# Kernel optimization log

Measured on AMD Instinct MI355X. Metric: run time of the kernel, lower is better.

The kernel has to match this reference:

```python
import jax, jax.numpy as jnp
import numpy as np

VOCAB = 50257
CH = 1024          # c_hidden_size = hidden_size(1020) + class_num(4)
LAT = 128
T = 1024
EOS = 1


def setup_inputs() -> dict:
    key = jax.random.key(0)
    ks = jax.random.split(key, 12)
    s = 0.02
    # tokens in [2, VOCAB) so EOS only appears at the final position
    toks = jax.random.randint(ks[0], (T,), 2, VOCAB, dtype=jnp.int32)
    input_tensor = toks.at[-1].set(EOS)
    inp = {
        "input_tensor": input_tensor,
        "h0": jnp.zeros((1, 1, CH), jnp.float32),
        "c0": jnp.zeros((1, 1, CH), jnp.float32),
        "eps": jax.random.normal(ks[1], (1, 1, LAT), jnp.float32),
        "emb": jax.random.normal(ks[2], (VOCAB, CH), jnp.float32) * s,
        "W_ih": jax.random.normal(ks[3], (4 * CH, CH), jnp.float32) * s,
        "W_hh": jax.random.normal(ks[4], (4 * CH, CH), jnp.float32) * s,
        "b_ih": jax.random.normal(ks[5], (4 * CH,), jnp.float32) * s,
        "b_hh": jax.random.normal(ks[6], (4 * CH,), jnp.float32) * s,
        "W_mean": jax.random.normal(ks[7], (LAT, 2 * CH), jnp.float32) * s,
        "b_mean": jnp.zeros((LAT,), jnp.float32),
        "W_logv": jax.random.normal(ks[8], (LAT, 2 * CH), jnp.float32) * s,
        "b_logv": jnp.zeros((LAT,), jnp.float32),
    }
    return inp


def reference(input_tensor, h0, c0, eps, emb, W_ih, W_hh, b_ih, b_hh,
              W_mean, b_mean, W_logv, b_logv):
    Tlen = input_tensor.shape[0]
    eos_idx = jnp.argmax(input_tensor == EOS)           # first EOS position
    active = jnp.arange(Tlen) < eos_idx                 # steps taken before break
    x_all = emb[input_tensor]                            # [T, CH]

    def step(carry, inp):
        h, c = carry
        x, a = inp
        gates = x @ W_ih.T + b_ih + h @ W_hh.T + b_hh    # [4*CH]
        i, f, g, o = jnp.split(gates, 4)                 # PyTorch LSTM gate order
        c_new = jax.nn.sigmoid(f) * c + jax.nn.sigmoid(i) * jnp.tanh(g)
        h_new = jax.nn.sigmoid(o) * jnp.tanh(c_new)
        h = jnp.where(a, h_new, h)
        c = jnp.where(a, c_new, c)
        return (h, c), None

    (h, c), _ = jax.lax.scan(step, (h0.reshape(-1), c0.reshape(-1)), (x_all, active))
    hc = jnp.concatenate([h, c])                         # cat((h, c), dim=2) flattened
    mean = hc @ W_mean.T + b_mean
    logv = hc @ W_logv.T + b_logv
    z = eps.reshape(-1) * jnp.exp(0.5 * logv) + mean     # reparameterize
    shp = (1, 1, LAT)
    return z.reshape(shp), mean.reshape(shp), logv.reshape(shp)
```

## Files before the change

### kernel.cpp

```cpp
#include <hip/hip_runtime.h>
#include <cstdint>
#include <cstddef>

#define T_LEN 1024
#define CH    1024
#define NGATE 4096
#define LAT   128
#define NBLK  128

#define WS_XG    0
#define WS_HBUF  (16777216)
#define WS_HFIN  (16777216 + 16384)
#define WS_CFIN  (16777216 + 24576)
#define WS_CTRL  (16777216 + 32768)

#define SWZ(i) ((i) ^ ((((i) >> 4) & 7) << 2))

__device__ __forceinline__ float sigmf(float x) { return 1.0f / (1.0f + expf(-x)); }

template <int CTRL, int RM>
__device__ __forceinline__ float dpp_add(float x) {
  int t = __builtin_amdgcn_update_dpp(0, __float_as_int(x), CTRL, RM, 0xf, true);
  return x + __int_as_float(t);
}

__device__ __forceinline__ float wave_sum63(float x) {
  x = dpp_add<0x111, 0xf>(x);
  x = dpp_add<0x112, 0xf>(x);
  x = dpp_add<0x114, 0xf>(x);
  x = dpp_add<0x118, 0xf>(x);
  x = dpp_add<0x142, 0xa>(x);
  x = dpp_add<0x143, 0xc>(x);
  return x;
}

__global__ __launch_bounds__(1024) void setup_k(const int* __restrict__ tok,
                                                int* __restrict__ ctrl) {
  __shared__ int red[1024];
  int tid = threadIdx.x;
  red[tid] = (tok[tid] == 1) ? tid : 0x7fffffff;
  __syncthreads();
  for (int s = 512; s > 0; s >>= 1) {
    if (tid < s) red[tid] = min(red[tid], red[tid + s]);
    __syncthreads();
  }
  if (tid == 0) {
    int e = red[0];
    ctrl[0] = (e == 0x7fffffff) ? 0 : e;
  }
}

__global__ __launch_bounds__(512) void xgemm_k(const int* __restrict__ tok,
                                               const float* __restrict__ emb,
                                               const float* __restrict__ Wih,
                                               const float* __restrict__ bih,
                                               const float* __restrict__ bhh,
                                               float* __restrict__ xg) {
  __shared__ float As[16 * 132];
  __shared__ float Bs[16 * 132];
  const int tid = threadIdx.x;
  const int r0 = blockIdx.x * 128;
  const int t0 = blockIdx.y * 128;
  const int tx = tid & 15, ty = tid >> 4;
  const int m0 = ty * 4, n0 = tx * 8;
  const int lrow = tid >> 2;
  const int kq   = (tid & 3) * 4;

  float acc[4][8];
#pragma unroll
  for (int i = 0; i < 4; i++)
#pragma unroll
    for (int j = 0; j < 8; j++) acc[i][j] = 0.0f;

  const int tokv = tok[t0 + lrow];
  const float* arow = emb + (size_t)tokv * CH;
  const float* brow = Wih + (size_t)(r0 + lrow) * CH;

  for (int k0 = 0; k0 < CH; k0 += 16) {
    float4 a4 = *(const float4*)(arow + k0 + kq);
    float4 b4 = *(const float4*)(brow + k0 + kq);
    __syncthreads();
    As[(kq + 0) * 132 + lrow] = a4.x;
    As[(kq + 1) * 132 + lrow] = a4.y;
    As[(kq + 2) * 132 + lrow] = a4.z;
    As[(kq + 3) * 132 + lrow] = a4.w;
    Bs[(kq + 0) * 132 + lrow] = b4.x;
    Bs[(kq + 1) * 132 + lrow] = b4.y;
    Bs[(kq + 2) * 132 + lrow] = b4.z;
    Bs[(kq + 3) * 132 + lrow] = b4.w;
    __syncthreads();
#pragma unroll
    for (int kk = 0; kk < 16; kk++) {
      float4 av = *(const float4*)&As[kk * 132 + m0];
      float4 b0 = *(const float4*)&Bs[kk * 132 + n0];
      float4 b1 = *(const float4*)&Bs[kk * 132 + n0 + 4];
      float aa[4] = {av.x, av.y, av.z, av.w};
      float bb[8] = {b0.x, b0.y, b0.z, b0.w, b1.x, b1.y, b1.z, b1.w};
#pragma unroll
      for (int i = 0; i < 4; i++)
#pragma unroll
        for (int j = 0; j < 8; j++) acc[i][j] += aa[i] * bb[j];
    }
  }

  float4 bi0 = *(const float4*)(bih + r0 + n0);
  float4 bi1 = *(const float4*)(bih + r0 + n0 + 4);
  float4 bh0 = *(const float4*)(bhh + r0 + n0);
  float4 bh1 = *(const float4*)(bhh + r0 + n0 + 4);
  float badd[8] = {bi0.x + bh0.x, bi0.y + bh0.y, bi0.z + bh0.z, bi0.w + bh0.w,
                   bi1.x + bh1.x, bi1.y + bh1.y, bi1.z + bh1.z, bi1.w + bh1.w};
#pragma unroll
  for (int i = 0; i < 4; i++) {
    float4 o0 = {acc[i][0] + badd[0], acc[i][1] + badd[1],
                 acc[i][2] + badd[2], acc[i][3] + badd[3]};
    float4 o1 = {acc[i][4] + badd[4], acc[i][5] + badd[5],
                 acc[i][6] + badd[6], acc[i][7] + badd[7]};
    float* dst = xg + (size_t)(t0 + m0 + i) * NGATE + r0 + n0;
    *(float4*)(dst) = o0;
    *(float4*)(dst + 4) = o1;
  }
}

__global__ __launch_bounds__(1024) void lstm_k(const float* __restrict__ h0,
                                               const float* __restrict__ c0,
                                               const float* __restrict__ eps,
                                               const float* __restrict__ Whh,
                                               const float* __restrict__ Wm,
                                               const float* __restrict__ bm,
                                               const float* __restrict__ Wl,
                                               const float* __restrict__ bl,
                                               const float* __restrict__ xg,
                                               unsigned long long* __restrict__ hbuf64,
                                               unsigned long long* __restrict__ hfin64,
                                               unsigned long long* __restrict__ cfin64,
                                               const int* __restrict__ ctrl,
                                               float* __restrict__ out) {
  __shared__ float hs[1024];
  __shared__ float hcs[2048];
  __shared__ float4 gpart[16];
  __shared__ float rs[32];

  const int tid = threadIdx.x;
  const int b = blockIdx.x;
  const int wv = tid >> 6;
  const int ln = tid & 63;
  const int dw = wv & 7;
  const int mb = (wv >> 3) * 2;
  const int hsw = SWZ(tid);
  const int swzmask = (ln & 7) << 2;
  const int idx0 = (ln * 16 + 4 * mb) ^ swzmask;
  const int idx1 = (ln * 16 + 4 * mb + 4) ^ swzmask;

  float4 w4[4][2];
#pragma unroll
  for (int q = 0; q < 4; q++) {
    const float* wr = Whh + (size_t)(q * 1024 + b * 8 + dw) * CH + ln * 16 + 4 * mb;
    w4[q][0] = *(const float4*)(wr);
    w4[q][1] = *(const float4*)(wr + 4);
  }

  const int eos = ctrl[0];

  float hreg = 0.0f, creg = 0.0f;
  if (tid < 8) { hreg = h0[b * 8 + tid]; creg = c0[b * 8 + tid]; }

  for (int t = 0; t < eos; t++) {
    float xq0 = 0.0f, xq1 = 0.0f, xq2 = 0.0f, xq3 = 0.0f;
    if (tid < 8) {
      const float* xp = xg + (size_t)t * NGATE + b * 8 + tid;
      xq0 = xp[0]; xq1 = xp[1024]; xq2 = xp[2048]; xq3 = xp[3072];
    }

    if (t == 0) {
      hs[hsw] = h0[tid];
    } else {
      const unsigned want = (unsigned)t;
      const unsigned long long* src = hbuf64 + (size_t)(t & 1) * 1024 + tid;
      unsigned long long v;
      do {
        v = __hip_atomic_load(src, __ATOMIC_RELAXED, __HIP_MEMORY_SCOPE_AGENT);
      } while ((unsigned)(v >> 32) != want);
      hs[hsw] = __uint_as_float((unsigned)(v & 0xffffffffu));
    }
    __syncthreads();

    float a0 = 0.0f, a1 = 0.0f, a2 = 0.0f, a3 = 0.0f;
    {
      const float4 h4a = *(const float4*)&hs[idx0];
      const float4 h4b = *(const float4*)&hs[idx1];
      a0 += w4[0][0].x * h4a.x; a0 += w4[0][0].y * h4a.y;
      a0 += w4[0][0].z * h4a.z; a0 += w4[0][0].w * h4a.w;
      a0 += w4[0][1].x * h4b.x; a0 += w4[0][1].y * h4b.y;
      a0 += w4[0][1].z * h4b.z; a0 += w4[0][1].w * h4b.w;
      a1 += w4[1][0].x * h4a.x; a1 += w4[1][0].y * h4a.y;
      a1 += w4[1][0].z * h4a.z; a1 += w4[1][0].w * h4a.w;
      a1 += w4[1][1].x * h4b.x; a1 += w4[1][1].y * h4b.y;
      a1 += w4[1][1].z * h4b.z; a1 += w4[1][1].w * h4b.w;
      a2 += w4[2][0].x * h4a.x; a2 += w4[2][0].y * h4a.y;
      a2 += w4[2][0].z * h4a.z; a2 += w4[2][0].w * h4a.w;
      a2 += w4[2][1].x * h4b.x; a2 += w4[2][1].y * h4b.y;
      a2 += w4[2][1].z * h4b.z; a2 += w4[2][1].w * h4b.w;
      a3 += w4[3][0].x * h4a.x; a3 += w4[3][0].y * h4a.y;
      a3 += w4[3][0].z * h4a.z; a3 += w4[3][0].w * h4a.w;
      a3 += w4[3][1].x * h4b.x; a3 += w4[3][1].y * h4b.y;
      a3 += w4[3][1].z * h4b.z; a3 += w4[3][1].w * h4b.w;
    }
    a0 = wave_sum63(a0);
    a1 = wave_sum63(a1);
    a2 = wave_sum63(a2);
    a3 = wave_sum63(a3);
    if (ln == 63) gpart[wv] = float4{a0, a1, a2, a3};
    __syncthreads();

    if (tid < 8) {
      const float4 g0 = gpart[tid];
      const float4 g1 = gpart[tid + 8];
      const float iv = g0.x + g1.x + xq0;
      const float fv = g0.y + g1.y + xq1;
      const float gg = g0.z + g1.z + xq2;
      const float ov = g0.w + g1.w + xq3;
      const float cn = sigmf(fv) * creg + sigmf(iv) * tanhf(gg);
      const float hn = sigmf(ov) * tanhf(cn);
      creg = cn; hreg = hn;
      const unsigned long long pv =
          ((unsigned long long)(unsigned)(t + 1) << 32) |
          (unsigned long long)__float_as_uint(hn);
      __hip_atomic_store(&hbuf64[(size_t)((t + 1) & 1) * 1024 + b * 8 + tid], pv,
                         __ATOMIC_RELAXED, __HIP_MEMORY_SCOPE_AGENT);
    }
  }

  if (tid < 8) {
    const unsigned long long ph = (1ull << 32) | (unsigned long long)__float_as_uint(hreg);
    const unsigned long long pc = (1ull << 32) | (unsigned long long)__float_as_uint(creg);
    __hip_atomic_store(&hfin64[b * 8 + tid], ph, __ATOMIC_RELAXED, __HIP_MEMORY_SCOPE_AGENT);
    __hip_atomic_store(&cfin64[b * 8 + tid], pc, __ATOMIC_RELAXED, __HIP_MEMORY_SCOPE_AGENT);
  }

  {
    unsigned long long vh, vc;
    do {
      vh = __hip_atomic_load(&hfin64[tid], __ATOMIC_RELAXED, __HIP_MEMORY_SCOPE_AGENT);
    } while ((unsigned)(vh >> 32) != 1u);
    do {
      vc = __hip_atomic_load(&cfin64[tid], __ATOMIC_RELAXED, __HIP_MEMORY_SCOPE_AGENT);
    } while ((unsigned)(vc >> 32) != 1u);
    hcs[tid] = __uint_as_float((unsigned)(vh & 0xffffffffu));
    hcs[1024 + tid] = __uint_as_float((unsigned)(vc & 0xffffffffu));
  }
  __syncthreads();

  float hc1 = hcs[tid];
  float hc2 = hcs[1024 + tid];
  float pm = Wm[(size_t)b * 2048 + tid] * hc1 + Wm[(size_t)b * 2048 + 1024 + tid] * hc2;
  float pl = Wl[(size_t)b * 2048 + tid] * hc1 + Wl[(size_t)b * 2048 + 1024 + tid] * hc2;
#pragma unroll
  for (int o = 32; o > 0; o >>= 1) {
    pm += __shfl_down(pm, o);
    pl += __shfl_down(pl, o);
  }
  if (ln == 0) { rs[wv] = pm; rs[16 + wv] = pl; }
  __syncthreads();
  if (tid == 0) {
    float m = 0.0f, l = 0.0f;
    for (int i = 0; i < 16; i++) { m += rs[i]; l += rs[16 + i]; }
    m += bm[b];
    l += bl[b];
    float z = eps[b] * expf(0.5f * l) + m;
    out[b] = z;
    out[LAT + b] = m;
    out[2 * LAT + b] = l;
  }
}

extern "C" void kernel_launch(void* const* d_in, const int* in_sizes, int n_in,
                              void* d_out, int out_size, void* d_ws, size_t ws_size,
                              hipStream_t stream) {
  const int*   tok = (const int*)d_in[0];
  const float* h0  = (const float*)d_in[1];
  const float* c0  = (const float*)d_in[2];
  const float* eps = (const float*)d_in[3];
  const float* emb = (const float*)d_in[4];
  const float* Wih = (const float*)d_in[5];
  const float* Whh = (const float*)d_in[6];
  const float* bih = (const float*)d_in[7];
  const float* bhh = (const float*)d_in[8];
  const float* Wm  = (const float*)d_in[9];
  const float* bm  = (const float*)d_in[10];
  const float* Wl  = (const float*)d_in[11];
  const float* bl  = (const float*)d_in[12];
  float* out = (float*)d_out;

  char* ws = (char*)d_ws;
  float* xg = (float*)(ws + WS_XG);
  unsigned long long* hbuf64 = (unsigned long long*)(ws + WS_HBUF);
  unsigned long long* hfin64 = (unsigned long long*)(ws + WS_HFIN);
  unsigned long long* cfin64 = (unsigned long long*)(ws + WS_CFIN);
  int* ctrl = (int*)(ws + WS_CTRL);

  setup_k<<<1, 1024, 0, stream>>>(tok, ctrl);
  xgemm_k<<<dim3(NGATE / 128, T_LEN / 128), 512, 0, stream>>>(tok, emb, Wih, bih, bhh, xg);

  void* args[] = {(void*)&h0, (void*)&c0, (void*)&eps, (void*)&Whh,
                  (void*)&Wm, (void*)&bm, (void*)&Wl, (void*)&bl,
                  (void*)&xg, (void*)&hbuf64, (void*)&hfin64, (void*)&cfin64,
                  (void*)&ctrl, (void*)&out};
  hipLaunchCooperativeKernel((void*)lstm_k, dim3(NBLK), dim3(1024), args, 0, stream);
}
```

Baseline: 2.494 ms.

## Pipeline h polling, use light barriers, fast gate math, retune LDS swizzle

```diff
diff --git a/kernel.cpp b/kernel.cpp
--- a/kernel.cpp
+++ b/kernel.cpp
@@ -14,7 +14,16 @@
 #define WS_CFIN  (16777216 + 24576)
 #define WS_CTRL  (16777216 + 32768)
 
-#define SWZ(i) ((i) ^ ((((i) >> 4) & 7) << 2))
+#define SWZ(j) ((j) ^ ((((j) >> 5) & 7) << 2))
+
+#define LOG2E 1.44269504088896340736f
+__device__ __forceinline__ float fsig(float x) {
+  return __builtin_amdgcn_rcpf(1.0f + __builtin_amdgcn_exp2f(-LOG2E * x));
+}
+__device__ __forceinline__ float ftanh(float x) {
+  float e = __builtin_amdgcn_exp2f(2.0f * LOG2E * x);
+  return 1.0f - 2.0f * __builtin_amdgcn_rcpf(e + 1.0f);
+}
 
 __device__ __forceinline__ float sigmf(float x) { return 1.0f / (1.0f + expf(-x)); }
 
@@ -32,6 +41,16 @@
   x = dpp_add<0x142, 0xa>(x);
   x = dpp_add<0x143, 0xc>(x);
   return x;
+}
+
+__device__ __forceinline__ void bar_lgkm() {
+  asm volatile("s_waitcnt lgkmcnt(0)" ::: "memory");
+  __builtin_amdgcn_s_barrier();
+  __builtin_amdgcn_sched_barrier(0);
+}
+
+__device__ __forceinline__ unsigned long long apoll(const unsigned long long* p) {
+  return __hip_atomic_load(p, __ATOMIC_RELAXED, __HIP_MEMORY_SCOPE_AGENT);
 }
 
 __global__ __launch_bounds__(1024) void setup_k(const int* __restrict__ tok,
@@ -147,7 +166,7 @@
   const int dw = wv & 7;
   const int mb = (wv >> 3) * 2;
   const int hsw = SWZ(tid);
-  const int swzmask = (ln & 7) << 2;
+  const int swzmask = ((ln >> 1) & 7) << 2;
   const int idx0 = (ln * 16 + 4 * mb) ^ swzmask;
   const int idx1 = (ln * 16 + 4 * mb + 4) ^ swzmask;
 
@@ -176,13 +195,22 @@
     } else {
       const unsigned want = (unsigned)t;
       const unsigned long long* src = hbuf64 + (size_t)(t & 1) * 1024 + tid;
-      unsigned long long v;
-      do {
-        v = __hip_atomic_load(src, __ATOMIC_RELAXED, __HIP_MEMORY_SCOPE_AGENT);
-      } while ((unsigned)(v >> 32) != want);
-      hs[hsw] = __uint_as_float((unsigned)(v & 0xffffffffu));
-    }
-    __syncthreads();
+      unsigned long long v0 = apoll(src), v1 = apoll(src),
+                         v2 = apoll(src), v3 = apoll(src);
+      unsigned long long got;
+      for (;;) {
+        if ((unsigned)(v0 >> 32) == want) { got = v0; break; }
+        v0 = apoll(src);
+        if ((unsigned)(v1 >> 32) == want) { got = v1; break; }
+        v1 = apoll(src);
+        if ((unsigned)(v2 >> 32) == want) { got = v2; break; }
+        v2 = apoll(src);
+        if ((unsigned)(v3 >> 32) == want) { got = v3; break; }
+        v3 = apoll(src);
+      }
+      hs[hsw] = __uint_as_float((unsigned)(got & 0xffffffffu));
+    }
+    bar_lgkm();
 
     float a0 = 0.0f, a1 = 0.0f, a2 = 0.0f, a3 = 0.0f;
     {
@@ -210,7 +238,7 @@
     a2 = wave_sum63(a2);
     a3 = wave_sum63(a3);
     if (ln == 63) gpart[wv] = float4{a0, a1, a2, a3};
-    __syncthreads();
+    bar_lgkm();
 
     if (tid < 8) {
       const float4 g0 = gpart[tid];
@@ -219,8 +247,8 @@
       const float fv = g0.y + g1.y + xq1;
       const float gg = g0.z + g1.z + xq2;
       const float ov = g0.w + g1.w + xq3;
-      const float cn = sigmf(fv) * creg + sigmf(iv) * tanhf(gg);
-      const float hn = sigmf(ov) * tanhf(cn);
+      const float cn = fsig(fv) * creg + fsig(iv) * ftanh(gg);
+      const float hn = fsig(ov) * ftanh(cn);
       creg = cn; hreg = hn;
       const unsigned long long pv =
           ((unsigned long long)(unsigned)(t + 1) << 32) |
```

New measurement: 2.761 ms. +10.7%, slower.
